# Performance work log

Hardware: AMD Instinct MI355X
Metric: run time of the kernel (lower is better)

The kernel has to match this reference:

```python
import jax, jax.numpy as jnp
import numpy as np

# Dimensions
BATCH = 4
NUM_NODE = 20000
NUM_EDGE = 1280000   # avg degree 64
K = 2                # num_rd_kernels
NUM_SEQ = 13         # num_sequence (13 time points -> 12 intervals)
SEQ_IN = 12
RES = 2              # fixed-step Euler substeps per interval (resolution)
TEMP = 1.0           # temperature for gate softmax
NUM_OUT = -12        # num_output_sequence slice


def setup_inputs() -> dict:
    key = jax.random.key(0)
    ks = jax.random.split(key, 6)
    inputs = jax.random.normal(ks[0], (BATCH, 1, NUM_NODE, SEQ_IN), dtype=jnp.float32)
    gate = jax.random.normal(ks[1], (NUM_SEQ - 1, K), dtype=jnp.float32)
    # edge list from adjacency CSV (from/to columns)
    src = jax.random.randint(ks[2], (NUM_EDGE,), 0, NUM_NODE)
    dst = jax.random.randint(ks[3], (NUM_EDGE,), 0, NUM_NODE)
    # learned per-kernel parameters of multi_reaction_diffusion
    w = jax.random.normal(ks[4], (K, NUM_EDGE), dtype=jnp.float32) * 0.1  # edge diffusivity logits
    r = jax.random.normal(ks[5], (K, NUM_NODE), dtype=jnp.float32) * 0.1  # node reaction coeffs
    return {"inputs": inputs, "gate": gate, "w": w, "r": r, "src": src, "dst": dst}


def _dxdt(x, g, w, r, src, dst):
    # x: [B,N]  g: [K]  w: [K,E]  r: [K,N]
    a = jax.nn.sigmoid(w)                                   # [K,E] edge diffusivity
    xs = x[:, src]                                          # [B,E]
    xd = x[:, dst]                                          # [B,E]
    msg = a[:, None, :] * (xs - xd)[None, :, :]             # [K,B,E]
    # scatter-add messages into destination nodes
    diff = jax.ops.segment_sum(jnp.moveaxis(msg, 2, 0), dst, num_segments=NUM_NODE)  # [N,K,B]
    diff = jnp.transpose(diff, (1, 2, 0))                   # [K,B,N]
    react = r[:, None, :] * x[None] * (1.0 - x[None])       # [K,B,N] logistic reaction
    return jnp.einsum('k,kbn->bn', g, diff + react)         # gate-weighted mix of RD kernels


def reference(inputs, gate, w, r, src, dst):
    x0 = inputs[:, 0, :, -1]                                # [B,N]
    dt = 1.0 / (NUM_SEQ - 1)
    h = jnp.float32(dt / RES)
    gates = jax.nn.softmax(gate / TEMP, axis=-1)            # [NUM_SEQ-1, K]

    def interval(x, g):
        def step(xc, _):
            return xc + h * _dxdt(xc, g, w, r, src, dst), None
        x, _ = jax.lax.scan(step, x, None, length=RES)
        return x, x

    _, traj = jax.lax.scan(interval, x0, gates)             # [NUM_SEQ-1, B, N]
    out = jnp.concatenate([x0[None], traj], axis=0)         # [NUM_SEQ, B, N]
    return out[NUM_OUT:]                                    # last 12 horizons
```

## Files before the change

kernel.cpp:

```cpp
#include <hip/hip_runtime.h>
#include <hip/hip_fp16.h>
#include <math.h>

#define NNODE 20000
#define NEDGE 1280000
#define HSTEP (1.0f/24.0f)
#define NBUCK 313
#define CAP   4608
#define EPB   2048

__global__ void rd_init(const float* __restrict__ inp,
                        float4* __restrict__ x,
                        int* __restrict__ cursor) {
    int n = blockIdx.x * blockDim.x + threadIdx.x;
    if (n < NBUCK) cursor[n] = n * CAP;
    if (n < NNODE) {
        float4 v;
        v.x = inp[0 * NNODE * 12 + n * 12 + 11];
        v.y = inp[1 * NNODE * 12 + n * 12 + 11];
        v.z = inp[2 * NNODE * 12 + n * 12 + 11];
        v.w = inp[3 * NNODE * 12 + n * 12 + 11];
        x[n] = v;
    }
}

__global__ __launch_bounds__(256) void rd_part(const int4* __restrict__ src4,
                                               const int4* __restrict__ dst4,
                                               const float4* __restrict__ w4,
                                               int* __restrict__ cursor,
                                               uint2* __restrict__ rec) {
    __shared__ int h[4][NBUCK];
    __shared__ uint4 cache[EPB / 4];
    int t = threadIdx.x, wv = t >> 6;
    for (int i = t; i < 4 * NBUCK; i += 256) ((int*)h)[i] = 0;
    __syncthreads();
    int q0 = blockIdx.x * (EPB / 4);
    #pragma unroll
    for (int k = 0; k < 2; ++k) {
        int qi = q0 + k * 256 + t;
        int4 d4 = dst4[qi];
        int dd[4] = {d4.x, d4.y, d4.z, d4.w};
        unsigned cc[4];
        #pragma unroll
        for (int u = 0; u < 4; ++u) {
            int rank = atomicAdd(&h[wv][dd[u] >> 6], 1);
            cc[u] = (unsigned)dd[u] | ((unsigned)rank << 15);
        }
        cache[k * 256 + t] = make_uint4(cc[0], cc[1], cc[2], cc[3]);
    }
    __syncthreads();
    for (int i = t; i < NBUCK; i += 256) {
        int c0 = h[0][i], c1 = h[1][i], c2 = h[2][i], c3 = h[3][i];
        int tot = c0 + c1 + c2 + c3;
        int gb = tot ? atomicAdd(&cursor[i], tot) : 0;
        h[0][i] = gb;
        h[1][i] = gb + c0;
        h[2][i] = gb + c0 + c1;
        h[3][i] = gb + c0 + c1 + c2;
    }
    __syncthreads();
    #pragma unroll
    for (int k = 0; k < 2; ++k) {
        int qi = q0 + k * 256 + t;
        int4 s4 = src4[qi];
        float4 wa = w4[qi];
        float4 wb = w4[NEDGE / 4 + qi];
        uint4 c4 = cache[k * 256 + t];
        int ss[4] = {s4.x, s4.y, s4.z, s4.w};
        float fa[4] = {wa.x, wa.y, wa.z, wa.w};
        float fb[4] = {wb.x, wb.y, wb.z, wb.w};
        unsigned cc[4] = {c4.x, c4.y, c4.z, c4.w};
        #pragma unroll
        for (int u = 0; u < 4; ++u) {
            int d = cc[u] & 0x7FFF;
            int rank = (int)(cc[u] >> 15);
            int b = d >> 6;
            int p = h[wv][b] + rank;
            float s0 = 1.0f / (1.0f + expf(-fa[u]));
            float s1 = 1.0f / (1.0f + expf(-fb[u]));
            __half2 hh = __floats2half2_rn(s0, s1);
            uint2 rq;
            rq.x = (unsigned)ss[u] | ((unsigned)(d & 63) << 16);
            rq.y = *(unsigned*)&hh;
            if (p < (b + 1) * CAP) rec[p] = rq;
        }
    }
}

__global__ void rd_bscan(const int* __restrict__ cursor, int* __restrict__ boff) {
    int lane = threadIdx.x;
    int carry = 0;
    #pragma unroll
    for (int c = 0; c < 5; ++c) {
        int i = c * 64 + lane;
        int v = (i < NBUCK) ? (cursor[i] - i * CAP) : 0;
        int incl = v;
        #pragma unroll
        for (int o = 1; o < 64; o <<= 1) {
            int u = __shfl_up(incl, o, 64);
            if (lane >= o) incl += u;
        }
        if (i < NBUCK) boff[i] = carry + incl - v;
        carry += __shfl(incl, 63, 64);
    }
    if (lane == 0) boff[NBUCK] = carry;
}

__global__ __launch_bounds__(512) void rd_bsort(const uint2* __restrict__ rec,
                                                const int* __restrict__ cursor,
                                                const int* __restrict__ boff,
                                                unsigned short* __restrict__ es16,
                                                unsigned* __restrict__ ew32,
                                                int* __restrict__ offsets) {
    __shared__ uint2 rs[CAP];
    __shared__ int h[64], excl[64];
    int b = blockIdx.x;
    int ib = b * CAP;
    int cnt = cursor[b] - ib; if (cnt > CAP) cnt = CAP;
    int ob = boff[b];
    if (threadIdx.x < 64) h[threadIdx.x] = 0;
    __syncthreads();
    for (int i = threadIdx.x; i < cnt; i += 512) {
        uint2 q = rec[ib + i];
        rs[i] = q;
        atomicAdd(&h[(q.x >> 16) & 63], 1);
    }
    __syncthreads();
    if (threadIdx.x < 64) {
        int lane = threadIdx.x;
        int v = h[lane];
        int incl = v;
        #pragma unroll
        for (int o = 1; o < 64; o <<= 1) {
            int u = __shfl_up(incl, o, 64);
            if (lane >= o) incl += u;
        }
        excl[lane] = incl - v;
        int n = b * 64 + lane;
        if (n < NNODE) offsets[n] = ob + excl[lane];
        h[lane] = 0;
    }
    if (b == NBUCK - 1 && threadIdx.x == 0) offsets[NNODE] = NEDGE;
    __syncthreads();
    for (int i = threadIdx.x; i < cnt; i += 512) {
        uint2 q = rs[i];
        int dl = (q.x >> 16) & 63;
        int rank = atomicAdd(&h[dl], 1);
        int p = ob + excl[dl] + rank;
        es16[p] = (unsigned short)(q.x & 0xFFFFu);
        ew32[p] = q.y;
    }
}

__global__ __launch_bounds__(256) void rd_step(
        const float4* __restrict__ xin, float4* __restrict__ xout,
        const unsigned short* __restrict__ es16,
        const unsigned* __restrict__ ew32,
        const int* __restrict__ offsets,
        const float* __restrict__ r, const float* __restrict__ gate,
        int itv, int write_out, float* __restrict__ out) {
    int tid  = blockIdx.x * 256 + threadIdx.x;
    int node = tid >> 4;
    int sub  = threadIdx.x & 15;
    float ga = gate[2 * itv], gb = gate[2 * itv + 1];
    float g0 = 1.0f / (1.0f + expf(gb - ga));
    float g1 = 1.0f - g0;

    int beg = offsets[node], end = offsets[node + 1];
    float4 xd = xin[node];
    float rc = fmaf(g0, r[node], g1 * r[NNODE + node]);

    float4 acc = make_float4(0.f, 0.f, 0.f, 0.f);
    float wsum = 0.f;
    int j = beg + sub;
    for (; j + 48 < end; j += 64) {
        unsigned a0 = es16[j], a1 = es16[j + 16], a2 = es16[j + 32], a3 = es16[j + 48];
        unsigned b0 = ew32[j], b1 = ew32[j + 16], b2 = ew32[j + 32], b3 = ew32[j + 48];
        float4 x0 = xin[a0], x1 = xin[a1], x2 = xin[a2], x3 = xin[a3];
        float2 f0 = __half22float2(*(__half2*)&b0);
        float2 f1 = __half22float2(*(__half2*)&b1);
        float2 f2 = __half22float2(*(__half2*)&b2);
        float2 f3 = __half22float2(*(__half2*)&b3);
        float we0 = fmaf(g0, f0.x, g1 * f0.y);
        float we1 = fmaf(g0, f1.x, g1 * f1.y);
        float we2 = fmaf(g0, f2.x, g1 * f2.y);
        float we3 = fmaf(g0, f3.x, g1 * f3.y);
        acc.x = fmaf(we0, x0.x, fmaf(we1, x1.x, fmaf(we2, x2.x, fmaf(we3, x3.x, acc.x))));
        acc.y = fmaf(we0, x0.y, fmaf(we1, x1.y, fmaf(we2, x2.y, fmaf(we3, x3.y, acc.y))));
        acc.z = fmaf(we0, x0.z, fmaf(we1, x1.z, fmaf(we2, x2.z, fmaf(we3, x3.z, acc.z))));
        acc.w = fmaf(we0, x0.w, fmaf(we1, x1.w, fmaf(we2, x2.w, fmaf(we3, x3.w, acc.w))));
        wsum += (we0 + we1) + (we2 + we3);
    }
    for (; j + 16 < end; j += 32) {
        unsigned a0 = es16[j], a1 = es16[j + 16];
        unsigned b0 = ew32[j], b1 = ew32[j + 16];
        float4 x0 = xin[a0], x1 = xin[a1];
        float2 f0 = __half22float2(*(__half2*)&b0);
        float2 f1 = __half22float2(*(__half2*)&b1);
        float we0 = fmaf(g0, f0.x, g1 * f0.y);
        float we1 = fmaf(g0, f1.x, g1 * f1.y);
        acc.x = fmaf(we0, x0.x, fmaf(we1, x1.x, acc.x));
        acc.y = fmaf(we0, x0.y, fmaf(we1, x1.y, acc.y));
        acc.z = fmaf(we0, x0.z, fmaf(we1, x1.z, acc.z));
        acc.w = fmaf(we0, x0.w, fmaf(we1, x1.w, acc.w));
        wsum += we0 + we1;
    }
    if (j < end) {
        unsigned a0 = es16[j];
        unsigned b0 = ew32[j];
        float4 x0 = xin[a0];
        float2 f0 = __half22float2(*(__half2*)&b0);
        float we0 = fmaf(g0, f0.x, g1 * f0.y);
        acc.x = fmaf(we0, x0.x, acc.x);
        acc.y = fmaf(we0, x0.y, acc.y);
        acc.z = fmaf(we0, x0.z, acc.z);
        acc.w = fmaf(we0, x0.w, acc.w);
        wsum += we0;
    }
    #pragma unroll
    for (int m = 8; m >= 1; m >>= 1) {
        acc.x += __shfl_xor(acc.x, m, 64);
        acc.y += __shfl_xor(acc.y, m, 64);
        acc.z += __shfl_xor(acc.z, m, 64);
        acc.w += __shfl_xor(acc.w, m, 64);
        wsum  += __shfl_xor(wsum,  m, 64);
    }
    float4 xn;
    xn.x = xd.x + HSTEP * ((acc.x - wsum * xd.x) + rc * xd.x * (1.0f - xd.x));
    xn.y = xd.y + HSTEP * ((acc.y - wsum * xd.y) + rc * xd.y * (1.0f - xd.y));
    xn.z = xd.z + HSTEP * ((acc.z - wsum * xd.z) + rc * xd.z * (1.0f - xd.z));
    xn.w = xd.w + HSTEP * ((acc.w - wsum * xd.w) + rc * xd.w * (1.0f - xd.w));
    if (sub == 0) xout[node] = xn;
    if (write_out && sub < 4) {
        float v = (sub == 0) ? xn.x : (sub == 1) ? xn.y : (sub == 2) ? xn.z : xn.w;
        out[(itv * 4 + sub) * NNODE + node] = v;
    }
}

extern "C" void kernel_launch(void* const* d_in, const int* in_sizes, int n_in,
                              void* d_out, int out_size, void* d_ws, size_t ws_size,
                              hipStream_t stream) {
    const float* inp  = (const float*)d_in[0];
    const float* gate = (const float*)d_in[1];
    const float* w    = (const float*)d_in[2];
    const float* r    = (const float*)d_in[3];
    const int*   src  = (const int*)d_in[4];
    const int*   dst  = (const int*)d_in[5];
    float* out = (float*)d_out;

    char* ws = (char*)d_ws;
    float4*         xA      = (float4*)(ws + 0);
    float4*         xB      = (float4*)(ws + 320512);
    int*            offsets = (int*)   (ws + 641024);
    int*            cursor  = (int*)   (ws + 721152);
    int*            boff    = (int*)   (ws + 722432);
    uint2*          rec     = (uint2*) (ws + 723712);
    unsigned short* es16    = (unsigned short*)(ws + 12262144);
    unsigned*       ew32    = (unsigned*)(ws + 14822144);

    rd_init <<<(NNODE + 255) / 256, 256, 0, stream>>>(inp, xA, cursor);
    rd_part <<<NEDGE / EPB, 256, 0, stream>>>((const int4*)src, (const int4*)dst,
                                              (const float4*)w, cursor, rec);
    rd_bscan<<<1, 64, 0, stream>>>(cursor, boff);
    rd_bsort<<<NBUCK, 512, 0, stream>>>(rec, cursor, boff, es16, ew32, offsets);

    float4* xin = xA;
    float4* xout = xB;
    for (int itv = 0; itv < 12; ++itv) {
        for (int s = 0; s < 2; ++s) {
            rd_step<<<NNODE * 16 / 256, 256, 0, stream>>>(xin, xout, es16, ew32,
                                                          offsets, r, gate, itv, s, out);
            float4* t = xin; xin = xout; xout = t;
        }
    }
}
```

Before: 252.4 us.

## Fuse all Euler steps into one persistent kernel with grid barrier

The 24 per-step launches are replaced by one persistent kernel of 625 blocks, 32 nodes each. Every block stages its slice of the CSR edge indices and half-precision weights in LDS once, then runs all steps, syncing through a two-level atomic grid barrier (groups of 25 blocks) in global memory. This removes launch overhead and repeated global reads of the edge arrays. It relies on all 625 blocks being co-resident, which risks deadlock otherwise. It also truncates the edge count at CAPB per block, which could silently drop edges for high-degree node groups.

```diff
diff --git a/kernel.cpp b/kernel.cpp
--- a/kernel.cpp
+++ b/kernel.cpp
@@ -8,12 +8,20 @@
 #define NBUCK 313
 #define CAP   4608
 #define EPB   2048
+#define NPB   32
+#define TPB   512
+#define NBLK  (NNODE/NPB)
+#define CAPB  2432
+#define NGRP  25
+#define GSZ   25
 
 __global__ void rd_init(const float* __restrict__ inp,
                         float4* __restrict__ x,
-                        int* __restrict__ cursor) {
+                        int* __restrict__ cursor,
+                        int* __restrict__ bar) {
     int n = blockIdx.x * blockDim.x + threadIdx.x;
     if (n < NBUCK) cursor[n] = n * CAP;
+    if (n < 1024) bar[n] = 0;
     if (n < NNODE) {
         float4 v;
         v.x = inp[0 * NNODE * 12 + n * 12 + 11];
@@ -152,88 +160,138 @@
     }
 }
 
-__global__ __launch_bounds__(256) void rd_step(
-        const float4* __restrict__ xin, float4* __restrict__ xout,
+__global__ __launch_bounds__(TPB, 6) void rd_run(
+        float4* __restrict__ xa, float4* __restrict__ xb,
         const unsigned short* __restrict__ es16,
         const unsigned* __restrict__ ew32,
         const int* __restrict__ offsets,
         const float* __restrict__ r, const float* __restrict__ gate,
-        int itv, int write_out, float* __restrict__ out) {
-    int tid  = blockIdx.x * 256 + threadIdx.x;
-    int node = tid >> 4;
-    int sub  = threadIdx.x & 15;
-    float ga = gate[2 * itv], gb = gate[2 * itv + 1];
-    float g0 = 1.0f / (1.0f + expf(gb - ga));
-    float g1 = 1.0f - g0;
-
-    int beg = offsets[node], end = offsets[node + 1];
-    float4 xd = xin[node];
-    float rc = fmaf(g0, r[node], g1 * r[NNODE + node]);
-
-    float4 acc = make_float4(0.f, 0.f, 0.f, 0.f);
-    float wsum = 0.f;
-    int j = beg + sub;
-    for (; j + 48 < end; j += 64) {
-        unsigned a0 = es16[j], a1 = es16[j + 16], a2 = es16[j + 32], a3 = es16[j + 48];
-        unsigned b0 = ew32[j], b1 = ew32[j + 16], b2 = ew32[j + 32], b3 = ew32[j + 48];
-        float4 x0 = xin[a0], x1 = xin[a1], x2 = xin[a2], x3 = xin[a3];
-        float2 f0 = __half22float2(*(__half2*)&b0);
-        float2 f1 = __half22float2(*(__half2*)&b1);
-        float2 f2 = __half22float2(*(__half2*)&b2);
-        float2 f3 = __half22float2(*(__half2*)&b3);
-        float we0 = fmaf(g0, f0.x, g1 * f0.y);
-        float we1 = fmaf(g0, f1.x, g1 * f1.y);
-        float we2 = fmaf(g0, f2.x, g1 * f2.y);
-        float we3 = fmaf(g0, f3.x, g1 * f3.y);
-        acc.x = fmaf(we0, x0.x, fmaf(we1, x1.x, fmaf(we2, x2.x, fmaf(we3, x3.x, acc.x))));
-        acc.y = fmaf(we0, x0.y, fmaf(we1, x1.y, fmaf(we2, x2.y, fmaf(we3, x3.y, acc.y))));
-        acc.z = fmaf(we0, x0.z, fmaf(we1, x1.z, fmaf(we2, x2.z, fmaf(we3, x3.z, acc.z))));
-        acc.w = fmaf(we0, x0.w, fmaf(we1, x1.w, fmaf(we2, x2.w, fmaf(we3, x3.w, acc.w))));
-        wsum += (we0 + we1) + (we2 + we3);
-    }
-    for (; j + 16 < end; j += 32) {
-        unsigned a0 = es16[j], a1 = es16[j + 16];
-        unsigned b0 = ew32[j], b1 = ew32[j + 16];
-        float4 x0 = xin[a0], x1 = xin[a1];
-        float2 f0 = __half22float2(*(__half2*)&b0);
-        float2 f1 = __half22float2(*(__half2*)&b1);
-        float we0 = fmaf(g0, f0.x, g1 * f0.y);
-        float we1 = fmaf(g0, f1.x, g1 * f1.y);
-        acc.x = fmaf(we0, x0.x, fmaf(we1, x1.x, acc.x));
-        acc.y = fmaf(we0, x0.y, fmaf(we1, x1.y, acc.y));
-        acc.z = fmaf(we0, x0.z, fmaf(we1, x1.z, acc.z));
-        acc.w = fmaf(we0, x0.w, fmaf(we1, x1.w, acc.w));
-        wsum += we0 + we1;
-    }
-    if (j < end) {
-        unsigned a0 = es16[j];
-        unsigned b0 = ew32[j];
-        float4 x0 = xin[a0];
-        float2 f0 = __half22float2(*(__half2*)&b0);
-        float we0 = fmaf(g0, f0.x, g1 * f0.y);
-        acc.x = fmaf(we0, x0.x, acc.x);
-        acc.y = fmaf(we0, x0.y, acc.y);
-        acc.z = fmaf(we0, x0.z, acc.z);
-        acc.w = fmaf(we0, x0.w, acc.w);
-        wsum += we0;
-    }
-    #pragma unroll
-    for (int m = 8; m >= 1; m >>= 1) {
-        acc.x += __shfl_xor(acc.x, m, 64);
-        acc.y += __shfl_xor(acc.y, m, 64);
-        acc.z += __shfl_xor(acc.z, m, 64);
-        acc.w += __shfl_xor(acc.w, m, 64);
-        wsum  += __shfl_xor(wsum,  m, 64);
-    }
-    float4 xn;
-    xn.x = xd.x + HSTEP * ((acc.x - wsum * xd.x) + rc * xd.x * (1.0f - xd.x));
-    xn.y = xd.y + HSTEP * ((acc.y - wsum * xd.y) + rc * xd.y * (1.0f - xd.y));
-    xn.z = xd.z + HSTEP * ((acc.z - wsum * xd.z) + rc * xd.z * (1.0f - xd.z));
-    xn.w = xd.w + HSTEP * ((acc.w - wsum * xd.w) + rc * xd.w * (1.0f - xd.w));
-    if (sub == 0) xout[node] = xn;
-    if (write_out && sub < 4) {
-        float v = (sub == 0) ? xn.x : (sub == 1) ? xn.y : (sub == 2) ? xn.z : xn.w;
-        out[(itv * 4 + sub) * NNODE + node] = v;
+        float* __restrict__ out, int* bar) {
+    __shared__ unsigned short les[CAPB];
+    __shared__ unsigned lew[CAPB];
+    __shared__ int lofs[NPB + 1];
+    __shared__ float lgate[24];
+    int t = threadIdx.x;
+    int n0 = blockIdx.x * NPB;
+    if (t <= NPB) lofs[t] = offsets[n0 + t];
+    if (t >= 64 && t < 88) lgate[t - 64] = gate[t - 64];
+    __syncthreads();
+    int ebase = lofs[0];
+    int ecnt  = lofs[NPB] - ebase; if (ecnt > CAPB) ecnt = CAPB;
+    for (int i = t; i < ecnt; i += TPB) {
+        les[i] = es16[ebase + i];
+        lew[i] = ew32[ebase + i];
+    }
+    int node = n0 + (t >> 4);
+    int sub  = t & 15;
+    float r0n = r[node], r1n = r[NNODE + node];
+    int jb = lofs[t >> 4] - ebase;
+    int je = lofs[(t >> 4) + 1] - ebase;
+    int grp = blockIdx.x / GSZ;
+    __syncthreads();
+
+    float4* xi = xa;
+    float4* xo = xb;
+    int phase = 0;
+    for (int itv = 0; itv < 12; ++itv) {
+        float ga = lgate[2 * itv], gb = lgate[2 * itv + 1];
+        float g0 = 1.0f / (1.0f + expf(gb - ga));
+        float g1 = 1.0f - g0;
+        float rc = fmaf(g0, r0n, g1 * r1n);
+        for (int s = 0; s < 2; ++s) {
+            float4 xd = xi[node];
+            float4 acc = make_float4(0.f, 0.f, 0.f, 0.f);
+            float wsum = 0.f;
+            int j = jb + sub;
+            for (; j + 48 < je; j += 64) {
+                unsigned a0 = les[j], a1 = les[j + 16], a2 = les[j + 32], a3 = les[j + 48];
+                unsigned b0 = lew[j], b1 = lew[j + 16], b2 = lew[j + 32], b3 = lew[j + 48];
+                float4 x0 = xi[a0], x1 = xi[a1], x2 = xi[a2], x3 = xi[a3];
+                float2 f0 = __half22float2(*(__half2*)&b0);
+                float2 f1 = __half22float2(*(__half2*)&b1);
+                float2 f2 = __half22float2(*(__half2*)&b2);
+                float2 f3 = __half22float2(*(__half2*)&b3);
+                float we0 = fmaf(g0, f0.x, g1 * f0.y);
+                float we1 = fmaf(g0, f1.x, g1 * f1.y);
+                float we2 = fmaf(g0, f2.x, g1 * f2.y);
+                float we3 = fmaf(g0, f3.x, g1 * f3.y);
+                acc.x = fmaf(we0, x0.x, fmaf(we1, x1.x, fmaf(we2, x2.x, fmaf(we3, x3.x, acc.x))));
+                acc.y = fmaf(we0, x0.y, fmaf(we1, x1.y, fmaf(we2, x2.y, fmaf(we3, x3.y, acc.y))));
+                acc.z = fmaf(we0, x0.z, fmaf(we1, x1.z, fmaf(we2, x2.z, fmaf(we3, x3.z, acc.z))));
+                acc.w = fmaf(we0, x0.w, fmaf(we1, x1.w, fmaf(we2, x2.w, fmaf(we3, x3.w, acc.w))));
+                wsum += (we0 + we1) + (we2 + we3);
+            }
+            for (; j + 16 < je; j += 32) {
+                unsigned a0 = les[j], a1 = les[j + 16];
+                unsigned b0 = lew[j], b1 = lew[j + 16];
+                float4 x0 = xi[a0], x1 = xi[a1];
+                float2 f0 = __half22float2(*(__half2*)&b0);
+                float2 f1 = __half22float2(*(__half2*)&b1);
+                float we0 = fmaf(g0, f0.x, g1 * f0.y);
+                float we1 = fmaf(g0, f1.x, g1 * f1.y);
+                acc.x = fmaf(we0, x0.x, fmaf(we1, x1.x, acc.x));
+                acc.y = fmaf(we0, x0.y, fmaf(we1, x1.y, acc.y));
+                acc.z = fmaf(we0, x0.z, fmaf(we1, x1.z, acc.z));
+                acc.w = fmaf(we0, x0.w, fmaf(we1, x1.w, acc.w));
+                wsum += we0 + we1;
+            }
+            if (j < je) {
+                unsigned a0 = les[j];
+                unsigned b0 = lew[j];
+                float4 x0 = xi[a0];
+                float2 f0 = __half22float2(*(__half2*)&b0);
+                float we0 = fmaf(g0, f0.x, g1 * f0.y);
+                acc.x = fmaf(we0, x0.x, acc.x);
+                acc.y = fmaf(we0, x0.y, acc.y);
+                acc.z = fmaf(we0, x0.z, acc.z);
+                acc.w = fmaf(we0, x0.w, acc.w);
+                wsum += we0;
+            }
+            #pragma unroll
+            for (int m = 8; m >= 1; m >>= 1) {
+                acc.x += __shfl_xor(acc.x, m, 64);
+                acc.y += __shfl_xor(acc.y, m, 64);
+                acc.z += __shfl_xor(acc.z, m, 64);
+                acc.w += __shfl_xor(acc.w, m, 64);
+                wsum  += __shfl_xor(wsum,  m, 64);
+            }
+            float4 xn;
+            xn.x = xd.x + HSTEP * ((acc.x - wsum * xd.x) + rc * xd.x * (1.0f - xd.x));
+            xn.y = xd.y + HSTEP * ((acc.y - wsum * xd.y) + rc * xd.y * (1.0f - xd.y));
+            xn.z = xd.z + HSTEP * ((acc.z - wsum * xd.z) + rc * xd.z * (1.0f - xd.z));
+            xn.w = xd.w + HSTEP * ((acc.w - wsum * xd.w) + rc * xd.w * (1.0f - xd.w));
+            if (sub == 0) xo[node] = xn;
+            if (s == 1 && sub < 4) {
+                float v = (sub == 0) ? xn.x : (sub == 1) ? xn.y : (sub == 2) ? xn.z : xn.w;
+                out[(itv * 4 + sub) * NNODE + node] = v;
+            }
+            ++phase;
+            if (phase < 24) {
+                __syncthreads();
+                if (t == 0) {
+                    int o1 = __hip_atomic_fetch_add(&bar[64 + grp * 32], 1,
+                                 __ATOMIC_ACQ_REL, __HIP_MEMORY_SCOPE_AGENT);
+                    bool released = false;
+                    if (o1 == phase * GSZ - 1) {
+                        int o0 = __hip_atomic_fetch_add(&bar[32], 1,
+                                     __ATOMIC_ACQ_REL, __HIP_MEMORY_SCOPE_AGENT);
+                        if (o0 == phase * NGRP - 1) {
+                            __hip_atomic_store(&bar[0], phase,
+                                __ATOMIC_RELEASE, __HIP_MEMORY_SCOPE_AGENT);
+                            released = true;
+                        }
+                    }
+                    if (!released) {
+                        while (__hip_atomic_load(&bar[0], __ATOMIC_RELAXED,
+                                                 __HIP_MEMORY_SCOPE_AGENT) < phase)
+                            __builtin_amdgcn_s_sleep(2);
+                        __builtin_amdgcn_fence(__ATOMIC_ACQUIRE, "agent");
+                    }
+                }
+                __syncthreads();
+            }
+            float4* tmp = xi; xi = xo; xo = tmp;
+        }
     }
 }
 
@@ -254,23 +312,15 @@
     int*            offsets = (int*)   (ws + 641024);
     int*            cursor  = (int*)   (ws + 721152);
     int*            boff    = (int*)   (ws + 722432);
-    uint2*          rec     = (uint2*) (ws + 723712);
-    unsigned short* es16    = (unsigned short*)(ws + 12262144);
-    unsigned*       ew32    = (unsigned*)(ws + 14822144);
-
-    rd_init <<<(NNODE + 255) / 256, 256, 0, stream>>>(inp, xA, cursor);
+    int*            bar     = (int*)   (ws + 723712);
+    uint2*          rec     = (uint2*) (ws + 727808);
+    unsigned short* es16    = (unsigned short*)(ws + 12266496);
+    unsigned*       ew32    = (unsigned*)(ws + 14826496);
+
+    rd_init <<<(NNODE + 255) / 256, 256, 0, stream>>>(inp, xA, cursor, bar);
     rd_part <<<NEDGE / EPB, 256, 0, stream>>>((const int4*)src, (const int4*)dst,
                                               (const float4*)w, cursor, rec);
     rd_bscan<<<1, 64, 0, stream>>>(cursor, boff);
     rd_bsort<<<NBUCK, 512, 0, stream>>>(rec, cursor, boff, es16, ew32, offsets);
-
-    float4* xin = xA;
-    float4* xout = xB;
-    for (int itv = 0; itv < 12; ++itv) {
-        for (int s = 0; s < 2; ++s) {
-            rd_step<<<NNODE * 16 / 256, 256, 0, stream>>>(xin, xout, es16, ew32,
-                                                          offsets, r, gate, itv, s, out);
-            float4* t = xin; xin = xout; xout = t;
-        }
-    }
-}
+    rd_run  <<<NBLK, TPB, 0, stream>>>(xA, xB, es16, ew32, offsets, r, gate, out, bar);
+}
```

Result: slower. 804.2 us (+218.6%).
